# Optimization experiments

Measured on AMD Instinct MI355X. Metric: run time of the kernel, lower is better.

## Reference

```python
import jax, jax.numpy as jnp
import numpy as np

# dims per init_kwargs
B, T, N = 2, 16, 8192
F0, F1, F2 = 4, 8, 8
K = 3
D0, D1 = 8, 4


def setup_inputs() -> dict:
    ks = jax.random.split(jax.random.key(0), 11)
    x = jax.random.normal(ks[0], (B, T, F0, N), jnp.float32)
    # GSO: random symmetric-ish shift operator, scaled for spectral stability
    S = jax.random.normal(ks[1], (N, N), jnp.float32) / np.float32(np.sqrt(N))
    h1 = jax.random.normal(ks[2], (F1, K, F0), jnp.float32) * 0.1   # layer-1 filter taps
    b1 = jax.random.normal(ks[3], (F1, 1), jnp.float32) * 0.1
    h2 = jax.random.normal(ks[4], (F2, K, F1), jnp.float32) * 0.1   # layer-2 filter taps
    b2 = jax.random.normal(ks[5], (F2, 1), jnp.float32) * 0.1
    W1 = jax.random.normal(ks[6], (D0, F2), jnp.float32) * 0.1      # readout Linear 1
    bw1 = jax.random.normal(ks[7], (D0,), jnp.float32) * 0.1
    W2 = jax.random.normal(ks[8], (D1, D0), jnp.float32) * 0.1      # readout Linear 2
    bw2 = jax.random.normal(ks[9], (D1,), jnp.float32) * 0.1
    return {"x": x, "S": S, "h1": h1, "b1": b1, "h2": h2, "b2": b2,
            "W1": W1, "bw1": bw1, "W2": W2, "bw2": bw2}


def graph_filter(x, S, h, b):
    # x: [B,T,Fin,N]; h: [Fout,K,Fin]; b: [Fout,1]
    # z_k = z_{k-1} @ S  (diffusion over node dim, LSIGF with E=1, no delay)
    taps = [x]
    for _ in range(h.shape[1] - 1):
        taps.append(jnp.matmul(taps[-1], S))
    z = jnp.stack(taps, axis=2)                       # [B,T,K,Fin,N]
    return jnp.einsum('gkf,btkfn->btgn', h, z) + b    # [B,T,Fout,N]


def reference(x, S, h1, b1, h2, b2, W1, bw1, W2, bw2):
    y = jnp.tanh(graph_filter(x, S, h1, b1))          # [B,T,F1,N]
    y = jnp.tanh(graph_filter(y, S, h2, b2))          # [B,T,F2,N]
    # per-node readout: Linear over feature axis
    y = jnp.swapaxes(y, 2, 3)                         # [B,T,N,F2]
    y = jnp.tanh(jnp.einsum('btnf,df->btnd', y, W1) + bw1)
    y = jnp.einsum('btnd,ed->btne', y, W2) + bw2
    return jnp.swapaxes(y, 2, 3)                      # [B,T,D1,N]
```

## Files before the change

### kernel.cpp

```cpp
#include <hip/hip_runtime.h>
#include <hip/hip_bf16.h>
#include <math.h>

constexpr int NN = 8192;

typedef short bh8 __attribute__((ext_vector_type(8)));
typedef float fl4 __attribute__((ext_vector_type(4)));

__device__ __forceinline__ float bf2f(ushort h) {
  return __uint_as_float(((uint)h) << 16);
}
__device__ __forceinline__ ushort f2bf(float f) {
  uint u = __float_as_uint(f);
  return (ushort)((u + 0x7fffu + ((u >> 16) & 1u)) >> 16);
}

constexpr size_t OFF_P  = 16;
constexpr size_t OFF_XC = 4096;
constexpr size_t OFF_Z1 = OFF_XC + 2097152;
constexpr size_t OFF_Y1 = OFF_Z1 + 2097152;
constexpr size_t OFF_V1 = OFF_Y1 + 4194304;
constexpr size_t OFF_CF = OFF_V1 + 4194304;
constexpr size_t OFF_ST = 33554432;

constexpr int PO_H1 = 0, PO_B1 = 96, PO_H2 = 104, PO_B2 = 296;
constexpr int PO_W1 = 304, PO_BW1 = 368, PO_W2 = 376, PO_BW2 = 408;

__global__ __launch_bounds__(256) void detect_convert(
    const ushort* __restrict__ Sraw,
    const void* h1, const void* b1, const void* h2, const void* b2,
    const void* W1, const void* bw1, const void* W2, const void* bw2,
    char* __restrict__ ws) {
  __shared__ int smax[256];
  __shared__ int sflag;
  const int t = threadIdx.x;
  int mx = 0;
  for (int k = 0; k < 32; ++k) {
    ushort u = Sraw[(size_t)(t * 32 + k) * 2];
    int e = (u >> 7) & 0xff;
    mx = mx > e ? mx : e;
  }
  smax[t] = mx;
  __syncthreads();
  for (int s = 128; s > 0; s >>= 1) {
    if (t < s) smax[t] = smax[t] > smax[t + s] ? smax[t] : smax[t + s];
    __syncthreads();
  }
  if (t == 0) {
    sflag = (smax[0] >= 0x90) ? 1 : 0;
    *(int*)ws = sflag;
  }
  __syncthreads();
  const int f32 = sflag;
  float* pb = (float*)(ws + OFF_P);
  const void* ptrs[8] = {h1, b1, h2, b2, W1, bw1, W2, bw2};
  const int offs[8] = {PO_H1, PO_B1, PO_H2, PO_B2, PO_W1, PO_BW1, PO_W2, PO_BW2};
  const int lens[8] = {96, 8, 192, 8, 64, 8, 32, 4};
  for (int idx = t; idx < 412; idx += 256) {
#pragma unroll
    for (int s = 0; s < 8; ++s) {
      if (idx >= offs[s] && idx < offs[s] + lens[s]) {
        const int j = idx - offs[s];
        pb[idx] = f32 ? ((const float*)ptrs[s])[j]
                      : bf2f(((const ushort*)ptrs[s])[j]);
      }
    }
  }
}

__global__ __launch_bounds__(256) void convert_x(const void* __restrict__ xraw,
                                                 const char* __restrict__ wsro,
                                                 ushort* __restrict__ xc) {
  const int f32 = *(const int*)wsro;
  const int i = (blockIdx.x * 256 + threadIdx.x) * 4;
  if (f32) {
    float4 v = *(const float4*)((const float*)xraw + i);
    uint2 o;
    o.x = (uint)f2bf(v.x) | ((uint)f2bf(v.y) << 16);
    o.y = (uint)f2bf(v.z) | ((uint)f2bf(v.w) << 16);
    *(uint2*)&xc[i] = o;
  } else {
    *(uint2*)&xc[i] = *(const uint2*)((const ushort*)xraw + i);
  }
}

__global__ __launch_bounds__(256) void cvt_f32_bf16(const float* __restrict__ src,
                                                    ushort* __restrict__ dst) {
  const int i = (blockIdx.x * 256 + threadIdx.x) * 4;
  float4 v = *(const float4*)&src[i];
  uint2 o;
  o.x = (uint)f2bf(v.x) | ((uint)f2bf(v.y) << 16);
  o.y = (uint)f2bf(v.z) | ((uint)f2bf(v.w) << 16);
  *(uint2*)&dst[i] = o;
}

__global__ __launch_bounds__(256) void transpose_k(const ushort* __restrict__ Sraw,
                                                   const char* __restrict__ wsro,
                                                   ushort* __restrict__ St) {
  __shared__ uint tileU[64][33];
  const int f32 = *(const int*)wsro;
  const int t = threadIdx.x;
  const int tn = blockIdx.x * 64;
  const int tk = blockIdx.y * 64;
  {
    const int kp = t >> 3;
    const int c  = (t & 7) * 8;
    if (f32) {
      const float* r0 = (const float*)Sraw + (size_t)(tk + 2 * kp) * NN + tn + c;
      float4 a0 = *(const float4*)r0;
      float4 a1 = *(const float4*)(r0 + 4);
      float4 b0 = *(const float4*)(r0 + NN);
      float4 b1 = *(const float4*)(r0 + NN + 4);
      tileU[c + 0][kp] = (uint)f2bf(a0.x) | ((uint)f2bf(b0.x) << 16);
      tileU[c + 1][kp] = (uint)f2bf(a0.y) | ((uint)f2bf(b0.y) << 16);
      tileU[c + 2][kp] = (uint)f2bf(a0.z) | ((uint)f2bf(b0.z) << 16);
      tileU[c + 3][kp] = (uint)f2bf(a0.w) | ((uint)f2bf(b0.w) << 16);
      tileU[c + 4][kp] = (uint)f2bf(a1.x) | ((uint)f2bf(b1.x) << 16);
      tileU[c + 5][kp] = (uint)f2bf(a1.y) | ((uint)f2bf(b1.y) << 16);
      tileU[c + 6][kp] = (uint)f2bf(a1.z) | ((uint)f2bf(b1.z) << 16);
      tileU[c + 7][kp] = (uint)f2bf(a1.w) | ((uint)f2bf(b1.w) << 16);
    } else {
      const ushort* r0 = Sraw + (size_t)(tk + 2 * kp) * NN + tn + c;
      uint4 ua = *(const uint4*)r0;
      uint4 ub = *(const uint4*)(r0 + NN);
      const ushort* ap = (const ushort*)&ua;
      const ushort* bp = (const ushort*)&ub;
#pragma unroll
      for (int j = 0; j < 8; ++j)
        tileU[c + j][kp] = (uint)ap[j] | ((uint)bp[j] << 16);
    }
  }
  __syncthreads();
  {
    const int n = t >> 2;
#pragma unroll
    for (int it = 0; it < 2; ++it) {
      const int q = (t & 3) + 4 * it;
      uint4 w;
      w.x = tileU[n][q * 4 + 0];
      w.y = tileU[n][q * 4 + 1];
      w.z = tileU[n][q * 4 + 2];
      w.w = tileU[n][q * 4 + 3];
      *(uint4*)&St[(size_t)(tn + n) * NN + tk + q * 8] = w;
    }
  }
}

template <int KR>
__global__ __launch_bounds__(512, 4) void gemm_t(const ushort* __restrict__ A,
                                                 const ushort* __restrict__ St,
                                                 float* __restrict__ CF) {
  __shared__ ushort As[2][128 * 64];
  __shared__ ushort Bs[2][128 * 64];
  const int tid = threadIdx.x;
  const int wave = tid >> 6, lane = tid & 63;
  const int lrow = lane & 15, quad = lane >> 4;
  const int m0 = blockIdx.y * 128;
  const int n0 = blockIdx.x * 128;
  const int kc0 = blockIdx.z * KR;
  const int wm = (wave & 1) * 64;
  const int wn = (wave >> 1) * 32;

  const int s0i = (wave * 2) * 64 + lane;
  const int s1i = (wave * 2 + 1) * 64 + lane;
  const int r0 = s0i >> 3, g0 = (s0i & 7) ^ (r0 & 7);
  const int r1 = s1i >> 3, g1 = (s1i & 7) ^ (r1 & 7);
  const ushort* a0p = A + (size_t)(m0 + r0) * NN + g0 * 8;
  const ushort* a1p = A + (size_t)(m0 + r1) * NN + g1 * 8;
  const ushort* b0p = St + (size_t)(n0 + r0) * NN + g0 * 8;
  const ushort* b1p = St + (size_t)(n0 + r1) * NN + g1 * 8;

  fl4 acc[4][2];
#pragma unroll
  for (int i = 0; i < 4; ++i)
#pragma unroll
    for (int j = 0; j < 2; ++j) acc[i][j] = (fl4){0.f, 0.f, 0.f, 0.f};

#define STAGE(buf, kc)                                                         \
  {                                                                            \
    __builtin_amdgcn_global_load_lds(                                          \
        (__attribute__((address_space(1))) void*)(a0p + (kc)),                 \
        (__attribute__((address_space(3))) void*)&As[buf][(wave * 2) * 512],   \
        16, 0, 0);                                                             \
    __builtin_amdgcn_global_load_lds(                                          \
        (__attribute__((address_space(1))) void*)(a1p + (kc)),                 \
        (__attribute__((address_space(3))) void*)&As[buf][(wave * 2 + 1) * 512],\
        16, 0, 0);                                                             \
    __builtin_amdgcn_global_load_lds(                                          \
        (__attribute__((address_space(1))) void*)(b0p + (kc)),                 \
        (__attribute__((address_space(3))) void*)&Bs[buf][(wave * 2) * 512],   \
        16, 0, 0);                                                             \
    __builtin_amdgcn_global_load_lds(                                          \
        (__attribute__((address_space(1))) void*)(b1p + (kc)),                 \
        (__attribute__((address_space(3))) void*)&Bs[buf][(wave * 2 + 1) * 512],\
        16, 0, 0);                                                             \
  }

#define COMPUTE(buf)                                                           \
  {                                                                            \
    _Pragma("unroll")                                                          \
    for (int is = 0; is < 2; ++is) {                                           \
      bh8 af[4], bf[2];                                                        \
      const int G = is * 4 + quad;                                             \
      _Pragma("unroll")                                                        \
      for (int i = 0; i < 4; ++i) {                                            \
        const int row = wm + i * 16 + lrow;                                    \
        af[i] = *(const bh8*)&As[buf][row * 64 + ((G ^ (row & 7)) * 8)];       \
      }                                                                        \
      _Pragma("unroll")                                                        \
      for (int j = 0; j < 2; ++j) {                                            \
        const int row = wn + j * 16 + lrow;                                    \
        bf[j] = *(const bh8*)&Bs[buf][row * 64 + ((G ^ (row & 7)) * 8)];       \
      }                                                                        \
      _Pragma("unroll")                                                        \
      for (int i = 0; i < 4; ++i)                                              \
        _Pragma("unroll")                                                      \
        for (int j = 0; j < 2; ++j)                                            \
          acc[i][j] = __builtin_amdgcn_mfma_f32_16x16x32_bf16(af[i], bf[j],    \
                                                              acc[i][j], 0, 0, 0); \
    }                                                                          \
  }

  STAGE(0, kc0)
  const int kend = kc0 + KR;
#pragma unroll 1
  for (int kc = kc0; kc < kend; kc += 128) {
    __syncthreads();
    STAGE(1, kc + 64)
    COMPUTE(0)
    __syncthreads();
    if (kc + 128 < kend) STAGE(0, kc + 128)
    COMPUTE(1)
  }
#undef STAGE
#undef COMPUTE

#pragma unroll
  for (int i = 0; i < 4; ++i)
#pragma unroll
    for (int j = 0; j < 2; ++j)
#pragma unroll
      for (int rr = 0; rr < 4; ++rr) {
        const int row = m0 + wm + i * 16 + quad * 4 + rr;
        const int col = n0 + wn + j * 16 + lrow;
        atomicAdd(&CF[(size_t)row * NN + col], acc[i][j][rr]);
      }
}

__global__ __launch_bounds__(256) void combine1(const ushort* __restrict__ xc,
                                                const ushort* __restrict__ z1,
                                                const float* __restrict__ z2f,
                                                const char* __restrict__ wsro,
                                                ushort* __restrict__ y1) {
  const float* pb = (const float*)(wsro + OFF_P);
  __shared__ float hs[96], bs[8];
  const int t = threadIdx.x;
  if (t < 96) hs[t] = pb[PO_H1 + t];
  if (t < 8) bs[t] = pb[PO_B1 + t];
  __syncthreads();
  const int idx = blockIdx.x * 256 + t;
  const int bt = idx >> 11;
  const int n4 = (idx & 2047) * 4;
  float acc[8][4];
#pragma unroll
  for (int g = 0; g < 8; ++g)
#pragma unroll
    for (int v = 0; v < 4; ++v) acc[g][v] = bs[g];
#pragma unroll
  for (int k = 0; k < 3; ++k)
#pragma unroll
    for (int f = 0; f < 4; ++f) {
      const size_t off = (size_t)(bt * 4 + f) * NN + n4;
      float val[4];
      if (k == 2) {
        float4 w = *(const float4*)&z2f[off];
        val[0] = w.x; val[1] = w.y; val[2] = w.z; val[3] = w.w;
      } else {
        const ushort* pp = (k == 0) ? xc : z1;
        uint2 w = *(const uint2*)&pp[off];
        val[0] = bf2f(w.x & 0xffff); val[1] = bf2f(w.x >> 16);
        val[2] = bf2f(w.y & 0xffff); val[3] = bf2f(w.y >> 16);
      }
#pragma unroll
      for (int g = 0; g < 8; ++g) {
        const float hw = hs[(g * 3 + k) * 4 + f];
#pragma unroll
        for (int v = 0; v < 4; ++v) acc[g][v] += hw * val[v];
      }
    }
#pragma unroll
  for (int g = 0; g < 8; ++g) {
    ushort o[4];
#pragma unroll
    for (int v = 0; v < 4; ++v) o[v] = f2bf(tanhf(acc[g][v]));
    uint2 w;
    w.x = (uint)o[0] | ((uint)o[1] << 16);
    w.y = (uint)o[2] | ((uint)o[3] << 16);
    *(uint2*)&y1[(size_t)(bt * 8 + g) * NN + n4] = w;
  }
}

__global__ __launch_bounds__(256) void combine2(const ushort* __restrict__ y1,
                                                const ushort* __restrict__ v1,
                                                const float* __restrict__ v2f,
                                                const char* __restrict__ wsro,
                                                void* __restrict__ outv) {
  const float* pb = (const float*)(wsro + OFF_P);
  const int f32 = *(const int*)wsro;
  __shared__ float h2s[192], W1s[64], W2s[32], b2s[8], bw1s[8], bw2s[4];
  const int t = threadIdx.x;
  if (t < 192) h2s[t] = pb[PO_H2 + t];
  if (t < 64) W1s[t] = pb[PO_W1 + t];
  if (t < 32) W2s[t] = pb[PO_W2 + t];
  if (t < 8) { b2s[t] = pb[PO_B2 + t]; bw1s[t] = pb[PO_BW1 + t]; }
  if (t < 4) bw2s[t] = pb[PO_BW2 + t];
  __syncthreads();
  const int idx = blockIdx.x * 256 + t;
  const int bt = idx >> 12;
  const int n2 = (idx & 4095) * 2;
  float acc[8][2];
#pragma unroll
  for (int g = 0; g < 8; ++g) { acc[g][0] = b2s[g]; acc[g][1] = b2s[g]; }
#pragma unroll
  for (int k = 0; k < 3; ++k)
#pragma unroll
    for (int g1 = 0; g1 < 8; ++g1) {
      const size_t off = (size_t)(bt * 8 + g1) * NN + n2;
      float v0, v1v;
      if (k == 2) {
        float2 w = *(const float2*)&v2f[off];
        v0 = w.x; v1v = w.y;
      } else {
        const ushort* pp = (k == 0) ? y1 : v1;
        uint w = *(const uint*)&pp[off];
        v0 = bf2f(w & 0xffff); v1v = bf2f(w >> 16);
      }
#pragma unroll
      for (int g2 = 0; g2 < 8; ++g2) {
        const float hw = h2s[(g2 * 3 + k) * 8 + g1];
        acc[g2][0] += hw * v0;
        acc[g2][1] += hw * v1v;
      }
    }
#pragma unroll
  for (int g = 0; g < 8; ++g) {
    acc[g][0] = tanhf(acc[g][0]);
    acc[g][1] = tanhf(acc[g][1]);
  }
  float o[4][2];
#pragma unroll
  for (int e = 0; e < 4; ++e) { o[e][0] = bw2s[e]; o[e][1] = bw2s[e]; }
#pragma unroll
  for (int d = 0; d < 8; ++d) {
    float s0 = bw1s[d], s1 = bw1s[d];
#pragma unroll
    for (int f = 0; f < 8; ++f) {
      const float w = W1s[d * 8 + f];
      s0 += w * acc[f][0];
      s1 += w * acc[f][1];
    }
    s0 = tanhf(s0);
    s1 = tanhf(s1);
#pragma unroll
    for (int e = 0; e < 4; ++e) {
      const float w = W2s[e * 8 + d];
      o[e][0] += w * s0;
      o[e][1] += w * s1;
    }
  }
#pragma unroll
  for (int e = 0; e < 4; ++e) {
    const size_t off = (size_t)(bt * 4 + e) * NN + n2;
    if (f32) {
      float2 w = {o[e][0], o[e][1]};
      *(float2*)&((float*)outv)[off] = w;
    } else {
      uint w = (uint)f2bf(o[e][0]) | ((uint)f2bf(o[e][1]) << 16);
      *(uint*)&((ushort*)outv)[off] = w;
    }
  }
}

extern "C" void kernel_launch(void* const* d_in, const int* in_sizes, int n_in,
                              void* d_out, int out_size, void* d_ws,
                              size_t ws_size, hipStream_t stream) {
  (void)in_sizes; (void)n_in; (void)out_size; (void)ws_size;
  const void* x = d_in[0];
  const ushort* S = (const ushort*)d_in[1];
  char* ws = (char*)d_ws;
  ushort* xc = (ushort*)(ws + OFF_XC);
  ushort* z1 = (ushort*)(ws + OFF_Z1);
  ushort* y1 = (ushort*)(ws + OFF_Y1);
  ushort* v1 = (ushort*)(ws + OFF_V1);
  float* CF = (float*)(ws + OFF_CF);
  ushort* St = (ushort*)(ws + OFF_ST);

  detect_convert<<<1, 256, 0, stream>>>(S, d_in[2], d_in[3], d_in[4], d_in[5],
                                        d_in[6], d_in[7], d_in[8], d_in[9], ws);
  convert_x<<<1024, 256, 0, stream>>>(x, ws, xc);
  transpose_k<<<dim3(128, 128), 256, 0, stream>>>(S, ws, St);

  hipMemsetAsync(CF, 0, 4194304, stream);
  gemm_t<1024><<<dim3(64, 1, 8), 512, 0, stream>>>(xc, St, CF);
  cvt_f32_bf16<<<1024, 256, 0, stream>>>(CF, z1);

  hipMemsetAsync(CF, 0, 4194304, stream);
  gemm_t<1024><<<dim3(64, 1, 8), 512, 0, stream>>>(z1, St, CF);
  combine1<<<256, 256, 0, stream>>>(xc, z1, CF, ws, y1);

  hipMemsetAsync(CF, 0, 8388608, stream);
  gemm_t<2048><<<dim3(64, 2, 4), 512, 0, stream>>>(y1, St, CF);
  cvt_f32_bf16<<<2048, 256, 0, stream>>>(CF, v1);

  hipMemsetAsync(CF, 0, 8388608, stream);
  gemm_t<2048><<<dim3(64, 2, 4), 512, 0, stream>>>(v1, St, CF);
  combine2<<<512, 256, 0, stream>>>(y1, v1, CF, ws, (void*)d_out);
}
```

Baseline: 653.3 us.

## Replace split-K atomics with per-slice partial buffers and deepen GEMM prefetch

The split-K GEMM now writes each K-slice's partial sums to its own fp32 buffer with plain stores instead of atomicAdd. The reduction is folded into the following convert and combine kernels, which also removes the memsets. The GEMM main loop now keeps two LDS stages in flight, using explicit vmcnt/lgkmcnt waits and raw s_barrier calls, so global loads overlap more with MFMA compute. In exchange there is extra partial-buffer traffic in the reduction kernels and a larger workspace, plus fragile hand-written waitcnt synchronization.

New measurement: 589.2 us. -9.8%, faster.

```diff
diff --git a/kernel.cpp b/kernel.cpp
--- a/kernel.cpp
+++ b/kernel.cpp
@@ -1,5 +1,4 @@
 #include <hip/hip_runtime.h>
-#include <hip/hip_bf16.h>
 #include <math.h>
 
 constexpr int NN = 8192;
@@ -20,8 +19,8 @@
 constexpr size_t OFF_Z1 = OFF_XC + 2097152;
 constexpr size_t OFF_Y1 = OFF_Z1 + 2097152;
 constexpr size_t OFF_V1 = OFF_Y1 + 4194304;
-constexpr size_t OFF_CF = OFF_V1 + 4194304;
 constexpr size_t OFF_ST = 33554432;
+constexpr size_t OFF_CF = 167772160;
 
 constexpr int PO_H1 = 0, PO_B1 = 96, PO_H2 = 104, PO_B2 = 296;
 constexpr int PO_W1 = 304, PO_BW1 = 368, PO_W2 = 376, PO_BW2 = 408;
@@ -84,13 +83,20 @@
   }
 }
 
-__global__ __launch_bounds__(256) void cvt_f32_bf16(const float* __restrict__ src,
-                                                    ushort* __restrict__ dst) {
-  const int i = (blockIdx.x * 256 + threadIdx.x) * 4;
-  float4 v = *(const float4*)&src[i];
+template <int Z>
+__global__ __launch_bounds__(256) void reduce_cvt(const float* __restrict__ src,
+                                                  size_t slice,
+                                                  ushort* __restrict__ dst) {
+  const size_t i = (size_t)(blockIdx.x * 256 + threadIdx.x) * 4;
+  float4 s = *(const float4*)&src[i];
+#pragma unroll
+  for (int z = 1; z < Z; ++z) {
+    float4 t = *(const float4*)&src[(size_t)z * slice + i];
+    s.x += t.x; s.y += t.y; s.z += t.z; s.w += t.w;
+  }
   uint2 o;
-  o.x = (uint)f2bf(v.x) | ((uint)f2bf(v.y) << 16);
-  o.y = (uint)f2bf(v.z) | ((uint)f2bf(v.w) << 16);
+  o.x = (uint)f2bf(s.x) | ((uint)f2bf(s.y) << 16);
+  o.y = (uint)f2bf(s.z) | ((uint)f2bf(s.w) << 16);
   *(uint2*)&dst[i] = o;
 }
 
@@ -160,6 +166,7 @@
   const int kc0 = blockIdx.z * KR;
   const int wm = (wave & 1) * 64;
   const int wn = (wave >> 1) * 32;
+  float* CP = CF + (size_t)blockIdx.z * (size_t)(gridDim.y * 128) * NN;
 
   const int s0i = (wave * 2) * 64 + lane;
   const int s1i = (wave * 2 + 1) * 64 + lane;
@@ -221,19 +228,40 @@
     }                                                                          \
   }
 
+#define BARRIER()                                                              \
+  {                                                                            \
+    asm volatile("" ::: "memory");                                             \
+    __builtin_amdgcn_s_barrier();                                              \
+    asm volatile("" ::: "memory");                                             \
+  }
+
   STAGE(0, kc0)
+  STAGE(1, kc0 + 64)
   const int kend = kc0 + KR;
 #pragma unroll 1
   for (int kc = kc0; kc < kend; kc += 128) {
-    __syncthreads();
-    STAGE(1, kc + 64)
+    asm volatile("s_waitcnt vmcnt(4)" ::: "memory");
+    BARRIER()
     COMPUTE(0)
-    __syncthreads();
-    if (kc + 128 < kend) STAGE(0, kc + 128)
+    asm volatile("s_waitcnt lgkmcnt(0)" ::: "memory");
+    BARRIER()
+    if (kc + 128 < kend) {
+      STAGE(0, kc + 128)
+      asm volatile("s_waitcnt vmcnt(4)" ::: "memory");
+    } else {
+      asm volatile("s_waitcnt vmcnt(0)" ::: "memory");
+    }
+    BARRIER()
     COMPUTE(1)
+    if (kc + 192 < kend) {
+      asm volatile("s_waitcnt lgkmcnt(0)" ::: "memory");
+      BARRIER()
+      STAGE(1, kc + 192)
+    }
   }
 #undef STAGE
 #undef COMPUTE
+#undef BARRIER
 
 #pragma unroll
   for (int i = 0; i < 4; ++i)
@@ -243,7 +271,7 @@
       for (int rr = 0; rr < 4; ++rr) {
         const int row = m0 + wm + i * 16 + quad * 4 + rr;
         const int col = n0 + wn + j * 16 + lrow;
-        atomicAdd(&CF[(size_t)row * NN + col], acc[i][j][rr]);
+        CP[(size_t)row * NN + col] = acc[i][j][rr];
       }
 }
 
@@ -274,6 +302,11 @@
       float val[4];
       if (k == 2) {
         float4 w = *(const float4*)&z2f[off];
+#pragma unroll
+        for (int z = 1; z < 8; ++z) {
+          float4 u = *(const float4*)&z2f[(size_t)z * 1048576 + off];
+          w.x += u.x; w.y += u.y; w.z += u.z; w.w += u.w;
+        }
         val[0] = w.x; val[1] = w.y; val[2] = w.z; val[3] = w.w;
       } else {
         const ushort* pp = (k == 0) ? xc : z1;
@@ -329,6 +362,11 @@
       float v0, v1v;
       if (k == 2) {
         float2 w = *(const float2*)&v2f[off];
+#pragma unroll
+        for (int z = 1; z < 4; ++z) {
+          float2 u = *(const float2*)&v2f[(size_t)z * 2097152 + off];
+          w.x += u.x; w.y += u.y;
+        }
         v0 = w.x; v1v = w.y;
       } else {
         const ushort* pp = (k == 0) ? y1 : v1;
@@ -400,19 +438,15 @@
   convert_x<<<1024, 256, 0, stream>>>(x, ws, xc);
   transpose_k<<<dim3(128, 128), 256, 0, stream>>>(S, ws, St);
 
-  hipMemsetAsync(CF, 0, 4194304, stream);
   gemm_t<1024><<<dim3(64, 1, 8), 512, 0, stream>>>(xc, St, CF);
-  cvt_f32_bf16<<<1024, 256, 0, stream>>>(CF, z1);
-
-  hipMemsetAsync(CF, 0, 4194304, stream);
+  reduce_cvt<8><<<1024, 256, 0, stream>>>(CF, (size_t)1048576, z1);
+
   gemm_t<1024><<<dim3(64, 1, 8), 512, 0, stream>>>(z1, St, CF);
   combine1<<<256, 256, 0, stream>>>(xc, z1, CF, ws, y1);
 
-  hipMemsetAsync(CF, 0, 8388608, stream);
   gemm_t<2048><<<dim3(64, 2, 4), 512, 0, stream>>>(y1, St, CF);
-  cvt_f32_bf16<<<2048, 256, 0, stream>>>(CF, v1);
-
-  hipMemsetAsync(CF, 0, 8388608, stream);
+  reduce_cvt<4><<<2048, 256, 0, stream>>>(CF, (size_t)2097152, v1);
+
   gemm_t<2048><<<dim3(64, 2, 4), 512, 0, stream>>>(v1, St, CF);
   combine2<<<512, 256, 0, stream>>>(y1, v1, CF, ws, (void*)d_out);
 }
```
